# Optimization experiments

Measured on AMD Instinct MI355X. Metric: run time of the kernel, lower is better.

The kernel has to match this reference:

```python
import jax, jax.numpy as jnp
import numpy as np

B, S, C = 1, 2048, 2048
H, D = 16, 128
FF = 8192
EPS = 1e-6


def _rms(x, w):
    return x * jax.lax.rsqrt(jnp.mean(x * x, axis=-1, keepdims=True) + EPS) * w


def _rope(x, cos, sin):
    # x: [B,S,H,D]; cos/sin: [S,D]
    x1, x2 = jnp.split(x, 2, axis=-1)
    rot = jnp.concatenate([-x2, x1], axis=-1)
    return x * cos[None, :, None, :] + rot * sin[None, :, None, :]


def setup_inputs() -> dict:
    key = jax.random.key(0)
    ks = jax.random.split(key, 12)
    # RoPE tables
    inv_freq = 1.0 / (10000.0 ** (jnp.arange(0, D, 2, dtype=jnp.float32) / D))
    freqs = jnp.arange(S, dtype=jnp.float32)[:, None] * inv_freq[None, :]
    emb = jnp.concatenate([freqs, freqs], axis=-1)  # [S,D]
    # causal additive mask
    causal = jnp.tril(jnp.ones((S, S), dtype=bool))
    mask = jnp.where(causal, 0.0, -1e9).astype(jnp.float32)[None, None]
    w = lambda k, shp: (jax.random.normal(k, shp, dtype=jnp.float32) * 0.02)
    return {
        "hidden_states": jax.random.normal(ks[0], (B, S, C), dtype=jnp.float32),
        "cos": jnp.cos(emb),
        "sin": jnp.sin(emb),
        "attention_mask": mask,
        "ln1_w": jnp.ones((C,), dtype=jnp.float32),
        "wq": w(ks[1], (C, C)),
        "wk": w(ks[2], (C, C)),
        "wv": w(ks[3], (C, C)),
        "wo": w(ks[4], (C, C)),
        "ln2_w": jnp.ones((C,), dtype=jnp.float32),
        "w_gate": w(ks[5], (FF, C)),
        "w_up": w(ks[6], (FF, C)),
        "w_down": w(ks[7], (C, FF)),
    }


def reference(hidden_states, cos, sin, attention_mask, ln1_w, wq, wk, wv, wo,
              ln2_w, w_gate, w_up, w_down):
    # --- input RMSNorm ---
    x = _rms(hidden_states, ln1_w)
    # --- W2 (Gaussian-kernel) attention ---
    q = (x @ wq.T).reshape(B, S, H, D)
    k = (x @ wk.T).reshape(B, S, H, D)
    v = (x @ wv.T).reshape(B, S, H, D)
    q = _rope(q, cos, sin).transpose(0, 2, 1, 3)  # [B,H,S,D]
    k = _rope(k, cos, sin).transpose(0, 2, 1, 3)
    v = v.transpose(0, 2, 1, 3)
    qk = jnp.einsum('bhid,bhjd->bhij', q, k)
    q2 = jnp.sum(q * q, axis=-1)  # [B,H,S]
    k2 = jnp.sum(k * k, axis=-1)
    dist2 = q2[..., :, None] - 2.0 * qk + k2[..., None, :]  # ||q-k||^2
    scores = -dist2 / (2.0 * np.sqrt(D).astype(np.float32)) + attention_mask
    attn = jax.nn.softmax(scores, axis=-1)
    ctx = jnp.einsum('bhij,bhjd->bhid', attn, v)
    attn_out = ctx.transpose(0, 2, 1, 3).reshape(B, S, C) @ wo.T
    h = hidden_states + attn_out
    # --- post-attn RMSNorm + SwiGLU FFN ---
    y = _rms(h, ln2_w)
    ffn = (jax.nn.silu(y @ w_gate.T) * (y @ w_up.T)) @ w_down.T
    return h + ffn
```

## Files before the change

### kernel.cpp

```cpp
#include <hip/hip_runtime.h>
#include <cstdint>
#include <cstddef>

typedef __bf16 bf16x8 __attribute__((ext_vector_type(8)));
typedef float f32x4 __attribute__((ext_vector_type(4)));

union V16 { uint4 u; bf16x8 b; unsigned short s[8]; };

__device__ __forceinline__ float b2f(unsigned short u) {
  unsigned int x = ((unsigned int)u) << 16;
  float f;
  __builtin_memcpy(&f, &x, 4);
  return f;
}
__device__ __forceinline__ unsigned short f2b(float f) {
  unsigned int u;
  __builtin_memcpy(&u, &f, 4);
  u = u + 0x7FFFu + ((u >> 16) & 1u);
  return (unsigned short)(u >> 16);
}

__device__ __forceinline__ f32x4 mfma16(bf16x8 a, bf16x8 b, f32x4 c) {
  return __builtin_amdgcn_mfma_f32_16x16x32_bf16(a, b, c, 0, 0, 0);
}

__device__ __forceinline__ void gld_lds16(const unsigned short* g, unsigned short* l) {
  __builtin_amdgcn_global_load_lds((__attribute__((address_space(1))) void*)g,
                                   (__attribute__((address_space(3))) void*)l,
                                   16, 0, 0);
}

__global__ __launch_bounds__(256) void cvt_all(const float* __restrict__ wq,
                                               const float* __restrict__ wk,
                                               const float* __restrict__ wv,
                                               const float* __restrict__ wo,
                                               const float* __restrict__ wg,
                                               const float* __restrict__ wu,
                                               const float* __restrict__ wd,
                                               unsigned short* __restrict__ dst) {
  const int b = blockIdx.x;
  const float* src;
  if (b < 16384) {
    const int w = b >> 12;
    src = (w == 0 ? wq : w == 1 ? wk : w == 2 ? wv : wo) + (size_t)(b & 4095) * 1024;
  } else if (b < 32768) {
    src = wg + (size_t)(b - 16384) * 1024;
  } else if (b < 49152) {
    src = wu + (size_t)(b - 32768) * 1024;
  } else {
    src = wd + (size_t)(b - 49152) * 1024;
  }
  const int o = threadIdx.x * 4;
  const float4 v = *(const float4*)(src + o);
  ushort4 r;
  r.x = f2b(v.x); r.y = f2b(v.y); r.z = f2b(v.z); r.w = f2b(v.w);
  *(ushort4*)(dst + (size_t)b * 1024 + o) = r;
}

__global__ __launch_bounds__(256) void rms_k(const float* __restrict__ xin,
                                             const float* __restrict__ wgt,
                                             unsigned short* __restrict__ out) {
  const int s = blockIdx.x;
  const int t = threadIdx.x;
  float vals[8];
  float ss = 0.f;
#pragma unroll
  for (int i = 0; i < 8; ++i) {
    const int c = t + i * 256;
    const float f = xin[(size_t)s * 2048 + c];
    vals[i] = f;
    ss += f * f;
  }
#pragma unroll
  for (int off = 32; off > 0; off >>= 1) ss += __shfl_xor(ss, off);
  __shared__ float red[4];
  if ((t & 63) == 0) red[t >> 6] = ss;
  __syncthreads();
  ss = red[0] + red[1] + red[2] + red[3];
  const float sc = rsqrtf(ss * (1.f / 2048.f) + 1e-6f);
#pragma unroll
  for (int i = 0; i < 8; ++i) {
    const int c = t + i * 256;
    out[(size_t)s * 2048 + c] = f2b(vals[i] * sc * wgt[c]);
  }
}

__global__ __launch_bounds__(256) void rope_qk(unsigned short* qb, unsigned short* kb,
                                               const float* __restrict__ cosb,
                                               const float* __restrict__ sinb,
                                               float* __restrict__ k2c) {
  const int idx = blockIdx.x * 256 + threadIdx.x;
  const int d = idx & 63;
  const int h = (idx >> 6) & 15;
  const int s = idx >> 10;
  const size_t base = (size_t)s * 2048 + h * 128;
  const int cb = s * 128;
  const float c1 = cosb[cb + d],      s1 = sinb[cb + d];
  const float c2 = cosb[cb + d + 64], s2 = sinb[cb + d + 64];
  {
    const float x1 = b2f(qb[base + d]), x2 = b2f(qb[base + d + 64]);
    qb[base + d]      = f2b(x1 * c1 - x2 * s1);
    qb[base + d + 64] = f2b(x2 * c2 + x1 * s2);
  }
  {
    const float x1 = b2f(kb[base + d]), x2 = b2f(kb[base + d + 64]);
    const float k1 = x1 * c1 - x2 * s1;
    const float k2 = x2 * c2 + x1 * s2;
    kb[base + d]      = f2b(k1);
    kb[base + d + 64] = f2b(k2);
    float ss = k1 * k1 + k2 * k2;
#pragma unroll
    for (int off = 32; off > 0; off >>= 1) ss += __shfl_xor(ss, off);
    if (d == 0) k2c[h * 2048 + s] = ss * 0.04419417382415922f;
  }
}

template <int EPI, int RT>
__global__ __launch_bounds__(256, 2) void gemm_nt(
    const unsigned short* __restrict__ A,
    const unsigned short* __restrict__ B0,
    const unsigned short* __restrict__ B1,
    const unsigned short* __restrict__ B2,
    unsigned short* C0, unsigned short* C1, unsigned short* C2,
    const float* auxf, float* Cf,
    int N, int K, int kstride) {
  constexpr int TM = RT * 32;
  constexpr int APASS = TM / 64;
  const unsigned short* B;
  unsigned short* C;
  size_t koff = 0;
  if constexpr (EPI == 0) {
    B = (blockIdx.z == 0) ? B0 : (blockIdx.z == 1 ? B1 : B2);
    C = (blockIdx.z == 0) ? C0 : (blockIdx.z == 1 ? C1 : C2);
  } else {
    B = B0;
    C = C0;
    if constexpr (EPI == 3) koff = (size_t)blockIdx.z * K;
  }

  const int m0 = blockIdx.y * TM;
  const int n0 = blockIdx.x * 128;
  const int t = threadIdx.x;
  const int lane = t & 63;
  const int w = t >> 6;
  const int quad = lane >> 4;
  const int l15 = lane & 15;
  const int wr = w >> 1;
  const int wc = w & 1;

  __shared__ __align__(16) unsigned short As[TM * 32];
  __shared__ __align__(16) unsigned short Bs[128 * 32];

  const f32x4 vzero = {0.f, 0.f, 0.f, 0.f};
  f32x4 acc[RT][4];
#pragma unroll
  for (int i = 0; i < RT; ++i)
#pragma unroll
    for (int j = 0; j < 4; ++j) acc[i][j] = vzero;

  const int srow = w * 16 + (lane >> 2);
  const int scol = (lane & 3) * 8;
  const unsigned short* Ag = A + (size_t)(m0 + srow) * kstride + scol + koff;
  const unsigned short* Bg = B + (size_t)(n0 + srow) * kstride + scol + koff;

  for (int k0 = 0; k0 < K; k0 += 32) {
#pragma unroll
    for (int p = 0; p < APASS; ++p)
      gld_lds16(Ag + (size_t)p * 64 * kstride + k0, As + p * 2048 + w * 512);
#pragma unroll
    for (int p = 0; p < 2; ++p)
      gld_lds16(Bg + (size_t)p * 64 * kstride + k0, Bs + p * 2048 + w * 512);
    __syncthreads();

    bf16x8 af[RT], bfr[4];
#pragma unroll
    for (int rt = 0; rt < RT; ++rt)
      af[rt] = *(const bf16x8*)&As[(wr * (RT * 16) + rt * 16 + l15) * 32 + quad * 8];
#pragma unroll
    for (int ct = 0; ct < 4; ++ct)
      bfr[ct] = *(const bf16x8*)&Bs[(wc * 64 + ct * 16 + l15) * 32 + quad * 8];
#pragma unroll
    for (int rt = 0; rt < RT; ++rt)
#pragma unroll
      for (int ct = 0; ct < 4; ++ct)
        acc[rt][ct] = mfma16(af[rt], bfr[ct], acc[rt][ct]);
    __syncthreads();
  }

  float* Cfz = Cf;
  if constexpr (EPI == 3)
    Cfz = Cf + (size_t)blockIdx.z * (size_t)gridDim.y * TM * N;

#pragma unroll
  for (int rt = 0; rt < RT; ++rt) {
#pragma unroll
    for (int ct = 0; ct < 4; ++ct) {
#pragma unroll
      for (int r = 0; r < 4; ++r) {
        const int m = m0 + wr * (RT * 16) + rt * 16 + quad * 4 + r;
        const int n = n0 + wc * 64 + ct * 16 + l15;
        const size_t idx = (size_t)m * N + n;
        const float a = acc[rt][ct][r];
        if constexpr (EPI == 0) {
          C[idx] = f2b(a);
        } else if constexpr (EPI == 1) {
          Cf[idx] = auxf[idx] + a;
        } else {
          Cfz[idx] = a;
        }
      }
    }
  }
}

#define BARRIER() asm volatile("s_barrier" ::: "memory")
#define WAITVM(N) asm volatile("s_waitcnt vmcnt(" #N ")" ::: "memory")
#define WAITLG()                                           \
  do {                                                     \
    asm volatile("s_waitcnt lgkmcnt(0)" ::: "memory");     \
    __builtin_amdgcn_sched_barrier(0);                     \
  } while (0)

#define LDA(BUF, KS, MQ)                                                       \
  _Pragma("unroll") for (int j = 0; j < 4; ++j)                                \
      afr[j] = *(const bf16x8*)(aB + (BUF) * 16384 + (KS) * 8192 +             \
                                ((MQ) * 64 + j * 16) * 32);

#define LDB(BUF, KS)                                                           \
  _Pragma("unroll") for (int nf = 0; nf < 4; ++nf)                             \
      bfr[nf] = *(const bf16x8*)(bB + (BUF) * 16384 + (KS) * 8192 +            \
                                 (nf * 16) * 32);

#define MF(MQ)                                                                 \
  do {                                                                         \
    __builtin_amdgcn_s_setprio(1);                                             \
    _Pragma("unroll") for (int j = 0; j < 4; ++j)                              \
    _Pragma("unroll") for (int nf = 0; nf < 4; ++nf)                           \
        acc[(MQ) * 4 + j][nf] = mfma16(afr[j], bfr[nf], acc[(MQ) * 4 + j][nf]);\
    __builtin_amdgcn_s_setprio(0);                                             \
  } while (0)

#define STA(BUF, KS)                                                           \
  do {                                                                         \
    unsigned short* d_ = AsB + (BUF) * 16384 + (KS) * 8192 + w * 512;          \
    gld_lds16(pA, d_);                                                         \
    gld_lds16(pA + (size_t)128 * kstr, d_ + 4096);                             \
    pA += 32;                                                                  \
  } while (0)

#define STB(BUF, KS)                                                           \
  do {                                                                         \
    unsigned short* d_ = BsB + (BUF) * 16384 + (KS) * 8192 + w * 512;          \
    gld_lds16(pB, d_);                                                         \
    gld_lds16(pB + (size_t)128 * kstr, d_ + 4096);                             \
    pB += 32;                                                                  \
  } while (0)

#define TILE_STEADY(P)                                                         \
  do {                                                                         \
    LDA(P, 0, 0); LDB(P, 0); STA((P) ^ 1, 1);                                  \
    BARRIER(); WAITLG(); MF(0); BARRIER();                                     \
    LDA(P, 0, 1);            STB((P) ^ 1, 1);                                  \
    BARRIER(); WAITLG(); MF(1); WAITVM(8); BARRIER();                          \
    LDA(P, 1, 0); LDB(P, 1); STA(P, 0);                                        \
    BARRIER(); WAITLG(); MF(0); BARRIER();                                     \
    LDA(P, 1, 1);            STB(P, 0);                                        \
    BARRIER(); WAITLG(); MF(1); WAITVM(8); BARRIER();                          \
  } while (0)

template <int EPI>
__global__ __launch_bounds__(512, 2) void gemm256(
    const unsigned short* __restrict__ A,
    const unsigned short* __restrict__ B,
    unsigned short* __restrict__ C0,
    unsigned short* __restrict__ C1,
    unsigned short* __restrict__ C2,
    float* __restrict__ Cf,
    int N, int kstr, int Ktiles) {
  const int gx = gridDim.x, gy = gridDim.y;
  const int nwg = gx * gy * gridDim.z;
  const int orig = blockIdx.x + gx * (blockIdx.y + gy * blockIdx.z);
  const int s = ((nwg & 7) == 0) ? ((orig & 7) * (nwg >> 3) + (orig >> 3)) : orig;
  const int bx = s % gx;
  const int sq = s / gx;
  const int by = sq % gy;
  const int bz = sq / gy;

  const int m0 = by * 256, n0 = bx * 256;
  const size_t koff = (size_t)bz * ((size_t)Ktiles * 64);

  const int t = threadIdx.x;
  const int lane = t & 63;
  const int w = t >> 6;
  const int quad = lane >> 4;
  const int l15 = lane & 15;
  const int wr = w >> 2;
  const int wc = w & 3;

  __shared__ __align__(16) unsigned short As[2][2][8192];
  __shared__ __align__(16) unsigned short Bs[2][2][8192];
  unsigned short* AsB = &As[0][0][0];
  unsigned short* BsB = &Bs[0][0][0];

  const f32x4 vzero = {0.f, 0.f, 0.f, 0.f};
  f32x4 acc[8][4];
#pragma unroll
  for (int i = 0; i < 8; ++i)
#pragma unroll
    for (int j = 0; j < 4; ++j) acc[i][j] = vzero;

  bf16x8 afr[4], bfr[4];

  const int ko = (quad ^ ((l15 >> 1) & 3)) * 8;
  const unsigned short* aB = AsB + wr * 4096 + l15 * 32 + ko;
  const unsigned short* bB = BsB + wc * 2048 + l15 * 32 + ko;

  const int usrc = (lane & 3) ^ ((lane >> 3) & 3);
  const unsigned short* pA =
      A + (size_t)(m0 + w * 16 + (lane >> 2)) * kstr + koff + usrc * 8;
  const unsigned short* pB =
      B + (size_t)(n0 + w * 16 + (lane >> 2)) * kstr + koff + usrc * 8;

  STA(0, 0); STB(0, 0);
  STA(0, 1); STB(0, 1);
  STA(1, 0); STB(1, 0);
  WAITVM(8);
  BARRIER();

  const int pairs = (Ktiles - 2) >> 1;
  for (int it = 0; it < pairs; ++it) {
    TILE_STEADY(0);
    TILE_STEADY(1);
  }
  LDA(0, 0, 0); LDB(0, 0); STA(1, 1);
  BARRIER(); WAITLG(); MF(0); BARRIER();
  LDA(0, 0, 1);            STB(1, 1);
  BARRIER(); WAITLG(); MF(1); WAITVM(8); BARRIER();
  LDA(0, 1, 0); LDB(0, 1);
  BARRIER(); WAITLG(); MF(0); BARRIER();
  LDA(0, 1, 1);
  BARRIER(); WAITLG(); MF(1); WAITVM(4); BARRIER();
  LDA(1, 0, 0); LDB(1, 0);
  BARRIER(); WAITLG(); MF(0); BARRIER();
  LDA(1, 0, 1);
  BARRIER(); WAITLG(); MF(1); WAITVM(0); BARRIER();
  LDA(1, 1, 0); LDB(1, 1);
  BARRIER(); WAITLG(); MF(0); BARRIER();
  LDA(1, 1, 1);
  BARRIER(); WAITLG(); MF(1);

  if constexpr (EPI == 2) {
    const size_t MN = (size_t)gy * 256 * N;
    float* Cp = Cf + (size_t)bz * MN;
#pragma unroll
    for (int mf = 0; mf < 8; ++mf) {
      const int m = m0 + wr * 128 + mf * 16 + quad * 4;
#pragma unroll
      for (int nf = 0; nf < 4; ++nf) {
        const int n = n0 + wc * 64 + nf * 16 + l15;
#pragma unroll
        for (int r = 0; r < 4; ++r) Cp[(size_t)(m + r) * N + n] = acc[mf][nf][r];
      }
    }
  } else {
    unsigned short* Cp;
    int nb;
    constexpr int ldc = (EPI == 0) ? 8192 : 2048;
    if constexpr (EPI == 0) {
      Cp = (n0 < 8192) ? C0 : C1;
      nb = n0 & 8191;
    } else {
      const int wsel = n0 >> 11;
      Cp = wsel == 0 ? C0 : (wsel == 1 ? C1 : C2);
      nb = n0 & 2047;
    }
#pragma unroll
    for (int mf = 0; mf < 8; ++mf) {
      const int m = m0 + wr * 128 + mf * 16 + quad * 4;
#pragma unroll
      for (int nf = 0; nf < 4; ++nf) {
        const int n = nb + wc * 64 + nf * 16 + l15;
#pragma unroll
        for (int r = 0; r < 4; ++r)
          Cp[(size_t)(m + r) * ldc + n] = f2b(acc[mf][nf][r]);
      }
    }
  }
}

__global__ __launch_bounds__(256) void silu_k(unsigned short* __restrict__ g,
                                              const unsigned short* __restrict__ u) {
  const size_t i = ((size_t)blockIdx.x * 256 + threadIdx.x) * 8;
  V16 gv, uv, ov;
  gv.u = *(const uint4*)(g + i);
  uv.u = *(const uint4*)(u + i);
#pragma unroll
  for (int e = 0; e < 8; ++e) {
    const float gf = b2f(gv.s[e]);
    const float uf = b2f(uv.s[e]);
    ov.s[e] = f2b(gf / (1.f + __expf(-gf)) * uf);
  }
  *(uint4*)(g + i) = ov.u;
}

__global__ __launch_bounds__(256) void comb4(const float* __restrict__ p,
                                             const float* __restrict__ hf,
                                             float* __restrict__ out) {
  const size_t i = ((size_t)blockIdx.x * 256 + threadIdx.x) * 4;
  const size_t MN = (size_t)2048 * 2048;
  float4 a = *(const float4*)(p + i);
  const float4 b = *(const float4*)(p + MN + i);
  const float4 c = *(const float4*)(p + 2 * MN + i);
  const float4 d = *(const float4*)(p + 3 * MN + i);
  const float4 h = *(const float4*)(hf + i);
  a.x += b.x + c.x + d.x + h.x;
  a.y += b.y + c.y + d.y + h.y;
  a.z += b.z + c.z + d.z + h.z;
  a.w += b.w + c.w + d.w + h.w;
  *(float4*)(out + i) = a;
}

__global__ __launch_bounds__(256, 3) void flash_w2(
    const unsigned short* __restrict__ q,
    const unsigned short* __restrict__ kk,
    const unsigned short* __restrict__ v,
    const float* __restrict__ k2c,
    unsigned short* __restrict__ ctx) {
  constexpr int Cw = 2048;
  constexpr float TWOC = 0.08838834764831843f;
  const int h = blockIdx.y;
  const int i = (h >= 8) ? (31 - blockIdx.x) : blockIdx.x;
  const int i0 = i * 64;
  const int t = threadIdx.x;
  const int lane = t & 63;
  const int w = t >> 6;
  const int quad = lane >> 4;
  const int l15 = lane & 15;

  __shared__ __align__(16) unsigned short Ks[64 * 136];
  __shared__ __align__(16) unsigned short VTs[128 * 72];
  __shared__ __align__(16) unsigned short Ps[4][16 * 72];

  bf16x8 aq[4];
  {
    const unsigned short* qp = q + (size_t)(i0 + w * 16 + l15) * Cw + h * 128;
#pragma unroll
    for (int kt = 0; kt < 4; ++kt) {
      V16 u;
      u.u = *(const uint4*)(qp + kt * 32 + quad * 8);
      aq[kt] = u.b;
    }
  }

  const f32x4 vzero = {0.f, 0.f, 0.f, 0.f};
  f32x4 o[8];
#pragma unroll
  for (int nt = 0; nt < 8; ++nt) o[nt] = vzero;
  float mrow[4] = {-1e30f, -1e30f, -1e30f, -1e30f};
  float lrow[4] = {0.f, 0.f, 0.f, 0.f};

  const int njt = i + 1;
  const int jr = t >> 2;
  const int c0 = (t & 3) * 32;
  const int jlo = jr & 7;
  const int jhi = jr >> 3;
  for (int jt = 0; jt < njt; ++jt) {
    const int j0 = jt * 64;
    __syncthreads();
    {
      const unsigned short* kp = kk + (size_t)(j0 + jr) * Cw + h * 128 + c0;
      const unsigned short* vp = v + (size_t)(j0 + jr) * Cw + h * 128 + c0;
#pragma unroll
      for (int ii = 0; ii < 4; ++ii) {
        *(uint4*)&Ks[jr * 136 + c0 + ii * 8] = *(const uint4*)(kp + ii * 8);
        V16 vu;
        vu.u = *(const uint4*)(vp + ii * 8);
#pragma unroll
        for (int e = 0; e < 8; ++e) {
          const int dd = c0 + ii * 8 + e;
          const int gs = (jhi ^ (dd >> 4)) & 7;
          VTs[dd * 72 + (jlo | (gs << 3))] = vu.s[e];
        }
      }
    }
    __syncthreads();

    float k2v[4];
#pragma unroll
    for (int ct = 0; ct < 4; ++ct) k2v[ct] = k2c[h * 2048 + j0 + ct * 16 + l15];

    f32x4 sc[4];
#pragma unroll
    for (int ct = 0; ct < 4; ++ct) {
      f32x4 a = vzero;
#pragma unroll
      for (int kt = 0; kt < 4; ++kt) {
        V16 u;
        u.u = *(const uint4*)&Ks[(ct * 16 + l15) * 136 + kt * 32 + quad * 8];
        a = mfma16(aq[kt], u.b, a);
      }
      sc[ct] = a;
    }

    const bool diag = (jt == njt - 1);
#pragma unroll
    for (int ct = 0; ct < 4; ++ct) {
#pragma unroll
      for (int r = 0; r < 4; ++r) {
        float s = fmaf(TWOC, sc[ct][r], -k2v[ct]);
        if (diag) {
          const int gi = w * 16 + quad * 4 + r;
          const int gj = ct * 16 + l15;
          s = (gj <= gi) ? s : -1e30f;
        }
        sc[ct][r] = s;
      }
    }

    float al[4];
#pragma unroll
    for (int r = 0; r < 4; ++r) {
      float rm = fmaxf(fmaxf(sc[0][r], sc[1][r]), fmaxf(sc[2][r], sc[3][r]));
      rm = fmaxf(rm, __shfl_xor(rm, 1));
      rm = fmaxf(rm, __shfl_xor(rm, 2));
      rm = fmaxf(rm, __shfl_xor(rm, 4));
      rm = fmaxf(rm, __shfl_xor(rm, 8));
      const float mn = fmaxf(mrow[r], rm);
      al[r] = __expf(mrow[r] - mn);
      mrow[r] = mn;
      float ps = 0.f;
#pragma unroll
      for (int ct = 0; ct < 4; ++ct) {
        const float p = __expf(sc[ct][r] - mn);
        sc[ct][r] = p;
        ps += p;
      }
      ps += __shfl_xor(ps, 1);
      ps += __shfl_xor(ps, 2);
      ps += __shfl_xor(ps, 4);
      ps += __shfl_xor(ps, 8);
      lrow[r] = lrow[r] * al[r] + ps;
    }
#pragma unroll
    for (int nt = 0; nt < 8; ++nt)
#pragma unroll
      for (int r = 0; r < 4; ++r) o[nt][r] *= al[r];

#pragma unroll
    for (int ct = 0; ct < 4; ++ct)
#pragma unroll
      for (int r = 0; r < 4; ++r)
        Ps[w][(quad * 4 + r) * 72 + ct * 16 + l15] = f2b(sc[ct][r]);

#pragma unroll
    for (int kt2 = 0; kt2 < 2; ++kt2) {
      V16 pa;
      pa.u = *(const uint4*)&Ps[w][l15 * 72 + kt2 * 32 + quad * 8];
#pragma unroll
      for (int nt = 0; nt < 8; ++nt) {
        V16 vb;
        const int dd = nt * 16 + l15;
        const int gs = (kt2 * 4 + quad) ^ nt;
        vb.u = *(const uint4*)&VTs[dd * 72 + gs * 8];
        o[nt] = mfma16(pa.b, vb.b, o[nt]);
      }
    }
  }

  float invl[4];
#pragma unroll
  for (int r = 0; r < 4; ++r) invl[r] = 1.f / lrow[r];
#pragma unroll
  for (int nt = 0; nt < 8; ++nt) {
#pragma unroll
    for (int r = 0; r < 4; ++r) {
      const int gi = i0 + w * 16 + quad * 4 + r;
      ctx[(size_t)gi * Cw + h * 128 + nt * 16 + l15] = f2b(o[nt][r] * invl[r]);
    }
  }
}

extern "C" void kernel_launch(void* const* d_in, const int* in_sizes, int n_in,
                              void* d_out, int out_size, void* d_ws, size_t ws_size,
                              hipStream_t stream) {
  (void)in_sizes; (void)n_in; (void)out_size; (void)ws_size;
  const float* hid  = (const float*)d_in[0];
  const float* cosb = (const float*)d_in[1];
  const float* sinb = (const float*)d_in[2];
  const float* ln1w = (const float*)d_in[4];
  const float* wq   = (const float*)d_in[5];
  const float* wk   = (const float*)d_in[6];
  const float* wv   = (const float*)d_in[7];
  const float* wo   = (const float*)d_in[8];
  const float* ln2w = (const float*)d_in[9];
  const float* wg   = (const float*)d_in[10];
  const float* wu   = (const float*)d_in[11];
  const float* wd   = (const float*)d_in[12];
  float* outp = (float*)d_out;

  const size_t SC = (size_t)2048 * 2048;
  const size_t FC = (size_t)8192 * 2048;
  unsigned short* p = (unsigned short*)d_ws;
  unsigned short* wqb = p;  p += SC;
  unsigned short* wkb = p;  p += SC;
  unsigned short* wvb = p;  p += SC;
  unsigned short* wob = p;  p += SC;
  unsigned short* wgb = p;  p += FC;
  unsigned short* wub = p;  p += FC;
  unsigned short* wdb = p;  p += FC;
  unsigned short* xn  = p;  p += SC;
  unsigned short* qb  = p;  p += SC;
  unsigned short* kb  = p;  p += SC;
  unsigned short* vb  = p;  p += SC;
  unsigned short* ctxb = p; p += SC;
  float* hf = (float*)p;   p += 2 * SC;
  float* k2cb = (float*)p;
  unsigned short* yn = xn;
  unsigned short* gate = wqb;
  unsigned short* upb  = qb;
  float* pd = (float*)wgb;

  cvt_all<<<65536, 256, 0, stream>>>(wq, wk, wv, wo, wg, wu, wd, wqb);

  rms_k<<<2048, 256, 0, stream>>>(hid, ln1w, xn);
  gemm256<1><<<dim3(24, 8, 1), 512, 0, stream>>>(xn, wqb, qb, kb, vb, nullptr,
                                                 6144, 2048, 32);
  rope_qk<<<8192, 256, 0, stream>>>(qb, kb, cosb, sinb, k2cb);
  flash_w2<<<dim3(32, 16), 256, 0, stream>>>(qb, kb, vb, k2cb, ctxb);
  gemm_nt<1, 2><<<dim3(16, 32, 1), 256, 0, stream>>>(ctxb, wob, wob, wob,
                                                     nullptr, nullptr, nullptr,
                                                     hid, hf, 2048, 2048, 2048);
  rms_k<<<2048, 256, 0, stream>>>(hf, ln2w, yn);
  gemm256<0><<<dim3(64, 8, 1), 512, 0, stream>>>(yn, wgb, gate, upb, nullptr, nullptr,
                                                 16384, 2048, 32);
  silu_k<<<8192, 256, 0, stream>>>(gate, upb);
  gemm256<2><<<dim3(8, 8, 4), 512, 0, stream>>>(gate, wdb, nullptr, nullptr, nullptr,
                                                pd, 2048, 8192, 32);
  comb4<<<4096, 256, 0, stream>>>(pd, hf, outp);
}
```

Measured before the change: 763.8 us.

## Double-buffer LDS fragment registers and drop per-quarter barriers in GEMM loop

The GEMM main loop now keeps two register sets for the A/B fragments, so the LDS reads for the next MFMA quarter are issued while the current quarter's MFMAs run. Most of the s_barriers between quarters are removed, leaving one mid-tile barrier and one at the end of each tile, and the vmcnt gates are retuned. The aim is to hide LDS latency and cut synchronisation stalls. In exchange the kernel needs more VGPRs, which could reduce occupancy at 512 threads with 2 blocks per CU, and the thinner barriers raise the risk of LDS read/write races.

```diff
diff --git a/kernel.cpp b/kernel.cpp
--- a/kernel.cpp
+++ b/kernel.cpp
@@ -221,22 +221,23 @@
     __builtin_amdgcn_sched_barrier(0);                     \
   } while (0)
 
-#define LDA(BUF, KS, MQ)                                                       \
-  _Pragma("unroll") for (int j = 0; j < 4; ++j)                                \
-      afr[j] = *(const bf16x8*)(aB + (BUF) * 16384 + (KS) * 8192 +             \
-                                ((MQ) * 64 + j * 16) * 32);
-
-#define LDB(BUF, KS)                                                           \
-  _Pragma("unroll") for (int nf = 0; nf < 4; ++nf)                             \
-      bfr[nf] = *(const bf16x8*)(bB + (BUF) * 16384 + (KS) * 8192 +            \
-                                 (nf * 16) * 32);
-
-#define MF(MQ)                                                                 \
+#define RD(SET, BUF, KS, MQ)                                                   \
+  do {                                                                         \
+    _Pragma("unroll") for (int j = 0; j < 4; ++j)                              \
+        afr##SET[j] = *(const bf16x8*)(aB + (BUF) * 16384 + (KS) * 8192 +      \
+                                       ((MQ) * 64 + j * 16) * 32);             \
+    _Pragma("unroll") for (int nf = 0; nf < 4; ++nf)                           \
+        bfr##SET[nf] = *(const bf16x8*)(bB + (BUF) * 16384 + (KS) * 8192 +     \
+                                        (nf * 16) * 32);                       \
+  } while (0)
+
+#define MFS(SET, MQ)                                                           \
   do {                                                                         \
     __builtin_amdgcn_s_setprio(1);                                             \
     _Pragma("unroll") for (int j = 0; j < 4; ++j)                              \
     _Pragma("unroll") for (int nf = 0; nf < 4; ++nf)                           \
-        acc[(MQ) * 4 + j][nf] = mfma16(afr[j], bfr[nf], acc[(MQ) * 4 + j][nf]);\
+        acc[(MQ) * 4 + j][nf] =                                                \
+            mfma16(afr##SET[j], bfr##SET[nf], acc[(MQ) * 4 + j][nf]);          \
     __builtin_amdgcn_s_setprio(0);                                             \
   } while (0)
 
@@ -256,16 +257,19 @@
     pB += 32;                                                                  \
   } while (0)
 
-#define TILE_STEADY(P)                                                         \
+#define NOSTG do {} while (0)
+
+#define TILE3(P, ST1, ST2, ST3, ST4, GATE)                                     \
   do {                                                                         \
-    LDA(P, 0, 0); LDB(P, 0); STA((P) ^ 1, 1);                                  \
-    BARRIER(); WAITLG(); MF(0); BARRIER();                                     \
-    LDA(P, 0, 1);            STB((P) ^ 1, 1);                                  \
-    BARRIER(); WAITLG(); MF(1); WAITVM(8); BARRIER();                          \
-    LDA(P, 1, 0); LDB(P, 1); STA(P, 0);                                        \
-    BARRIER(); WAITLG(); MF(0); BARRIER();                                     \
-    LDA(P, 1, 1);            STB(P, 0);                                        \
-    BARRIER(); WAITLG(); MF(1); WAITVM(8); BARRIER();                          \
+    RD(A, P, 0, 0); ST1;                                                       \
+    WAITLG(); MFS(A, 0); RD(B, P, 0, 1);                                       \
+    ST2;                                                                       \
+    WAITLG(); MFS(B, 1); RD(A, P, 1, 0);                                       \
+    BARRIER(); ST3;                                                            \
+    WAITLG(); MFS(A, 0); RD(B, P, 1, 1);                                       \
+    ST4;                                                                       \
+    WAITLG(); MFS(B, 1);                                                       \
+    GATE; BARRIER();                                                           \
   } while (0)
 
 template <int EPI>
@@ -309,7 +313,7 @@
 #pragma unroll
     for (int j = 0; j < 4; ++j) acc[i][j] = vzero;
 
-  bf16x8 afr[4], bfr[4];
+  bf16x8 afrA[4], bfrA[4], afrB[4], bfrB[4];
 
   const int ko = (quad ^ ((l15 >> 1) & 3)) * 8;
   const unsigned short* aB = AsB + wr * 4096 + l15 * 32 + ko;
@@ -324,30 +328,16 @@
   STA(0, 0); STB(0, 0);
   STA(0, 1); STB(0, 1);
   STA(1, 0); STB(1, 0);
-  WAITVM(8);
+  WAITVM(4);
   BARRIER();
 
   const int pairs = (Ktiles - 2) >> 1;
   for (int it = 0; it < pairs; ++it) {
-    TILE_STEADY(0);
-    TILE_STEADY(1);
-  }
-  LDA(0, 0, 0); LDB(0, 0); STA(1, 1);
-  BARRIER(); WAITLG(); MF(0); BARRIER();
-  LDA(0, 0, 1);            STB(1, 1);
-  BARRIER(); WAITLG(); MF(1); WAITVM(8); BARRIER();
-  LDA(0, 1, 0); LDB(0, 1);
-  BARRIER(); WAITLG(); MF(0); BARRIER();
-  LDA(0, 1, 1);
-  BARRIER(); WAITLG(); MF(1); WAITVM(4); BARRIER();
-  LDA(1, 0, 0); LDB(1, 0);
-  BARRIER(); WAITLG(); MF(0); BARRIER();
-  LDA(1, 0, 1);
-  BARRIER(); WAITLG(); MF(1); WAITVM(0); BARRIER();
-  LDA(1, 1, 0); LDB(1, 1);
-  BARRIER(); WAITLG(); MF(0); BARRIER();
-  LDA(1, 1, 1);
-  BARRIER(); WAITLG(); MF(1);
+    TILE3(0, STA(1, 1), STB(1, 1), STA(0, 0), STB(0, 0), WAITVM(4));
+    TILE3(1, STA(0, 1), STB(0, 1), STA(1, 0), STB(1, 0), WAITVM(4));
+  }
+  TILE3(0, STA(1, 1), STB(1, 1), NOSTG, NOSTG, WAITVM(0));
+  TILE3(1, NOSTG, NOSTG, NOSTG, NOSTG, NOSTG);
 
   if constexpr (EPI == 2) {
     const size_t MN = (size_t)gy * 256 * N;
```

After: 761.9 us. No clear change (-0.3%).
